# Performance work log

Measured on AMD Instinct MI355X. Metric: run time of the kernel, lower is better.

The kernel has to match this reference:

```python
import jax, jax.numpy as jnp
import numpy as np

N = 50000          # nodes
E = 400000         # edges
F = 128            # num_embeddings
NUM_TYPES = 100    # num_atoms (embedding vocab)
CUTOFF = 5.0
N_RBF = 20


def _silu(x):
    return x * jax.nn.sigmoid(x)


def setup_inputs() -> dict:
    key = jax.random.key(0)
    ks = jax.random.split(key, 16)
    pos = jax.random.normal(ks[0], (N, 3), dtype=jnp.float32) * 3.0
    z = jax.random.randint(ks[1], (N,), 0, NUM_TYPES)
    dst = jax.random.randint(ks[2], (E,), 0, N)
    # ensure src != dst so distances are nonzero
    src = (dst + 1 + jax.random.randint(ks[3], (E,), 0, N - 1)) % N
    def lin(k, fan_in, fan_out):
        kw, kb = jax.random.split(k)
        lim = 1.0 / np.sqrt(fan_in)
        W = jax.random.uniform(kw, (fan_out, fan_in), minval=-lim, maxval=lim, dtype=jnp.float32)
        b = jax.random.uniform(kb, (fan_out,), minval=-lim, maxval=lim, dtype=jnp.float32)
        return W, b
    emb_table = jax.random.normal(ks[4], (NUM_TYPES, F), dtype=jnp.float32)
    Wp1, bp1 = lin(ks[5], F, F)
    Wp2, bp2 = lin(ks[6], F, 3 * F)
    Ww, bw = lin(ks[7], N_RBF, 3 * F)
    Wu, bu = lin(ks[8], F, F)
    Wv, bv = lin(ks[9], F, F)
    Wu1, bu1 = lin(ks[10], 2 * F, F)
    Wu2, bu2 = lin(ks[11], F, 3 * F)
    return dict(pos=pos, emb_table=emb_table,
                Wp1=Wp1, bp1=bp1, Wp2=Wp2, bp2=bp2, Ww=Ww, bw=bw,
                Wu=Wu, bu=bu, Wv=Wv, bv=bv, Wu1=Wu1, bu1=bu1, Wu2=Wu2, bu2=bu2,
                z=z, src=src, dst=dst)


def painn_forward(pos, emb_table, Wp1, bp1, Wp2, bp2, Ww, bw, Wu, bu, Wv, bv,
                  Wu1, bu1, Wu2, bu2, z, src, dst):
    s = emb_table[z]                                  # [N,F] scalar features
    v = jnp.zeros((N, F, 3), dtype=s.dtype)          # equivariant features

    # ---- message block ----
    phi = _silu(s @ Wp1.T + bp1) @ Wp2.T + bp2       # [N,3F]
    rel = pos[dst] - pos[src]                        # [E,3]
    d = jnp.maximum(jnp.linalg.norm(rel, axis=-1), 1e-9)  # [E]
    n = jnp.arange(1, N_RBF + 1, dtype=jnp.float32)
    rbf = jnp.sin(n * jnp.pi * d[:, None] / CUTOFF) / d[:, None]   # [E,20]
    Wf = rbf @ Ww.T + bw                             # [E,3F]
    split = phi[src] * Wf                            # [E,3F] gated message
    ds = jax.ops.segment_sum(split[:, :F], dst, num_segments=N)    # [N,F]
    direction = rel / d[:, None]                     # [E,3]
    dv_e = v[src] * split[:, F:2 * F, None] + split[:, 2 * F:, None] * direction[:, None, :]  # [E,F,3]
    dv = jax.ops.segment_sum(dv_e, dst, num_segments=N)            # [N,F,3]
    s = s + ds
    v = v + dv

    # ---- update block ----
    U = jnp.einsum('nfc,gf->ngc', v, Wu) + bu[:, None]   # [N,F,3]
    V = jnp.einsum('nfc,gf->ngc', v, Wv) + bv[:, None]   # [N,F,3]
    Vn = jnp.linalg.norm(V, axis=-1)                     # [N,F]
    h = jnp.concatenate([s, Vn], axis=-1)                # [N,2F]
    a = _silu(h @ Wu1.T + bu1) @ Wu2.T + bu2             # [N,3F]
    dv2 = U * a[:, :F, None]                             # [N,F,3]
    ds2 = a[:, F:2 * F] + jnp.sum(U * V, axis=-1) * a[:, 2 * F:]   # [N,F]
    return s + ds2, v + dv2


def reference(pos, emb_table, Wp1, bp1, Wp2, bp2, Ww, bw, Wu, bu, Wv, bv,
              Wu1, bu1, Wu2, bu2, z, src, dst):
    return painn_forward(pos, emb_table, Wp1, bp1, Wp2, bp2, Ww, bw, Wu, bu,
                         Wv, bv, Wu1, bu1, Wu2, bu2, z, src, dst)
```

## Files before the change

kernel.cpp:

```cpp
#include <hip/hip_runtime.h>

#define NN 50000
#define EE 400000
#define FF 128
#define NRBF 20
#define MAXDEG 64
#define PI_OVER_CUT 0.6283185307179586f

typedef _Float16 h8 __attribute__((ext_vector_type(8)));
typedef float    f4 __attribute__((ext_vector_type(4)));

union pk32 { unsigned int u; _Float16 h[2]; };

__global__ __launch_bounds__(256) void k_zero(int* __restrict__ counts) {
    int i = blockIdx.x * 256 + threadIdx.x;
    if (i < NN) counts[i] = 0;
}

__global__ __launch_bounds__(256) void k_bucket(const int* __restrict__ dst,
                                                int* __restrict__ counts,
                                                int* __restrict__ slots) {
    int e = blockIdx.x * 256 + threadIdx.x;
    if (e < EE) {
        int n = dst[e];
        int slot = atomicAdd(&counts[n], 1);
        if (slot < MAXDEG) slots[n * MAXDEG + slot] = e;
    }
}

__global__ __launch_bounds__(256) void k_wconv(
    const float* __restrict__ Wu, const float* __restrict__ Wv,
    const float* __restrict__ Wu1, const float* __restrict__ Wu2,
    const float* __restrict__ Wp1, const float* __restrict__ Wp2,
    const float* __restrict__ Ww, const float* __restrict__ bw,
    _Float16* __restrict__ Wuh, _Float16* __restrict__ Wvh,
    _Float16* __restrict__ Wu1h, _Float16* __restrict__ Wu2h,
    _Float16* __restrict__ Wp1h, _Float16* __restrict__ Wp2h,
    _Float16* __restrict__ Wwh32)
{
    int i = blockIdx.x * 256 + threadIdx.x;
    if (i < 16384) { Wuh[i] = (_Float16)Wu[i]; Wvh[i] = (_Float16)Wv[i];
                     Wp1h[i] = (_Float16)Wp1[i]; }
    if (i < 32768) { Wu1h[i] = (_Float16)Wu1[i]; }
    if (i < 49152) { Wu2h[i] = (_Float16)Wu2[i]; Wp2h[i] = (_Float16)Wp2[i]; }
    if (i < 8192) {
        int col = i >> 5, k = i & 31;
        int sr = col < 128 ? col : col + 128;
        _Float16 v = (_Float16)0.f;
        if (k < 20)       v = (_Float16)Ww[sr * NRBF + k];
        else if (k == 20) v = (_Float16)bw[sr];
        Wwh32[i] = v;
    }
}

__global__ __launch_bounds__(256) void k_node_phi_mfma(
    const float* __restrict__ emb, const int* __restrict__ z,
    const _Float16* __restrict__ Wp1h, const float* __restrict__ bp1,
    const _Float16* __restrict__ Wp2h, const float* __restrict__ bp2,
    unsigned int* __restrict__ phi_pk, float* __restrict__ s_io)
{
    __shared__ _Float16 Ss[32 * 128];
    __shared__ _Float16 H1s[32 * 128];

    const int t    = threadIdx.x;
    const int lane = t & 63;
    const int w    = t >> 6;
    const int lr   = lane & 15;
    const int lq   = lane >> 4;
    const int n0   = blockIdx.x * 32;
    const f4 z4 = {0.f, 0.f, 0.f, 0.f};

    for (int i = t; i < 512; i += 256) {
        int n = i >> 4, gr = i & 15;
        int nn = n0 + n; if (nn > NN - 1) nn = NN - 1;
        const float* sp = &emb[(size_t)z[nn] * FF + gr * 8];
        float4 aa = *(const float4*)sp;
        float4 bb = *(const float4*)(sp + 4);
        h8 hv;
        hv[0] = (_Float16)aa.x; hv[1] = (_Float16)aa.y;
        hv[2] = (_Float16)aa.z; hv[3] = (_Float16)aa.w;
        hv[4] = (_Float16)bb.x; hv[5] = (_Float16)bb.y;
        hv[6] = (_Float16)bb.z; hv[7] = (_Float16)bb.w;
        *(h8*)&Ss[(n * 16 + (gr ^ (n & 15))) * 8] = hv;
        float* op = &s_io[(size_t)nn * FF + gr * 8];
        *(float4*)op       = aa;
        *(float4*)(op + 4) = bb;
    }
    __syncthreads();

    f4 acc1[2][2];
    #pragma unroll
    for (int a = 0; a < 2; ++a)
        #pragma unroll
        for (int m = 0; m < 2; ++m) acc1[a][m] = z4;
    {
        const _Float16* bb = Wp1h + (size_t)lr * 128 + lq * 8;
        #pragma unroll
        for (int g2 = 0; g2 < 2; ++g2) {
            h8 bf[4];
            #pragma unroll
            for (int ks = 0; ks < 4; ++ks)
                bf[ks] = *(const h8*)(bb + ((2 * w + g2) * 16) * 128 + ks * 32);
            #pragma unroll
            for (int mt = 0; mt < 2; ++mt) {
                const int r = mt * 16 + lr;
                #pragma unroll
                for (int ks = 0; ks < 4; ++ks) {
                    h8 af = *(const h8*)&Ss[(r * 16 + ((ks * 4 + lq) ^ (r & 15))) * 8];
                    acc1[g2][mt] = __builtin_amdgcn_mfma_f32_16x16x32_f16(
                        af, bf[ks], acc1[g2][mt], 0, 0, 0);
                }
            }
        }
    }
    #pragma unroll
    for (int g2 = 0; g2 < 2; ++g2) {
        const int g = (2 * w + g2) * 16 + lr;
        const float b1 = bp1[g];
        #pragma unroll
        for (int mt = 0; mt < 2; ++mt)
            #pragma unroll
            for (int r = 0; r < 4; ++r) {
                float x = acc1[g2][mt][r] + b1;
                float y = x / (1.f + __expf(-x));
                int n = mt * 16 + lq * 4 + r;
                H1s[(n * 16 + ((g >> 3) ^ (n & 15))) * 8 + (g & 7)] = (_Float16)y;
            }
    }
    __syncthreads();

    f4 accS[2][2], accV[2][2];
    #pragma unroll
    for (int a = 0; a < 2; ++a)
        #pragma unroll
        for (int m = 0; m < 2; ++m) { accS[a][m] = z4; accV[a][m] = z4; }
    {
        const _Float16* bbs = Wp2h + (size_t)lr * 128 + lq * 8;
        const _Float16* bbv = Wp2h + (size_t)(256 + lr) * 128 + lq * 8;
        #pragma unroll
        for (int g2 = 0; g2 < 2; ++g2) {
            h8 bfs[4], bfv[4];
            #pragma unroll
            for (int ks = 0; ks < 4; ++ks) {
                bfs[ks] = *(const h8*)(bbs + ((2 * w + g2) * 16) * 128 + ks * 32);
                bfv[ks] = *(const h8*)(bbv + ((2 * w + g2) * 16) * 128 + ks * 32);
            }
            #pragma unroll
            for (int mt = 0; mt < 2; ++mt) {
                const int r = mt * 16 + lr;
                #pragma unroll
                for (int ks = 0; ks < 4; ++ks) {
                    h8 af = *(const h8*)&H1s[(r * 16 + ((ks * 4 + lq) ^ (r & 15))) * 8];
                    accS[g2][mt] = __builtin_amdgcn_mfma_f32_16x16x32_f16(
                        af, bfs[ks], accS[g2][mt], 0, 0, 0);
                    accV[g2][mt] = __builtin_amdgcn_mfma_f32_16x16x32_f16(
                        af, bfv[ks], accV[g2][mt], 0, 0, 0);
                }
            }
        }
    }
    #pragma unroll
    for (int g2 = 0; g2 < 2; ++g2) {
        const int g = (2 * w + g2) * 16 + lr;
        const float bsa = bp2[g], bva = bp2[256 + g];
        #pragma unroll
        for (int mt = 0; mt < 2; ++mt)
            #pragma unroll
            for (int r = 0; r < 4; ++r) {
                int n = mt * 16 + lq * 4 + r;
                int nn = n0 + n;
                if (nn < NN) {
                    pk32 pk;
                    pk.h[0] = (_Float16)(accS[g2][mt][r] + bsa);
                    pk.h[1] = (_Float16)(accV[g2][mt][r] + bva);
                    phi_pk[(size_t)nn * FF + g] = pk.u;
                }
            }
    }
}

__global__ __launch_bounds__(128) void k_edge_mfma(
    const float* __restrict__ pos,
    const _Float16* __restrict__ Wwh32,
    const int* __restrict__ src,
    const int* __restrict__ counts, const int* __restrict__ slots,
    const unsigned int* __restrict__ phi_pk,
    float* __restrict__ s_io,
    _Float16* __restrict__ xg)
{
    __shared__ _Float16 A[16 * 32];
    __shared__ float dirs[16][4];
    __shared__ float dls[16];
    __shared__ unsigned int wf[16 * 130];

    const int t    = threadIdx.x;
    const int lane = t & 63;
    const int w    = t >> 6;
    const int lr   = lane & 15;
    const int lq   = lane >> 4;
    const int n    = blockIdx.x;
    const f4 z4 = {0.f, 0.f, 0.f, 0.f};

    h8 bf[8];
    #pragma unroll
    for (int j = 0; j < 8; ++j)
        bf[j] = *(const h8*)&Wwh32[(size_t)((w * 8 + j) * 16 + lr) * 32 + lq * 8];

    const float px = pos[3 * n], py = pos[3 * n + 1], pz = pos[3 * n + 2];

    int deg = counts[n];
    deg = deg > MAXDEG ? MAXDEG : deg;

    float acc_s = 0.f, av0 = 0.f, av1 = 0.f, av2 = 0.f;

    for (int t0 = 0; t0 < deg; t0 += 16) {
        const int degT = (deg - t0) < 16 ? (deg - t0) : 16;
        __syncthreads();
        if (t < degT) {
            int e  = slots[n * MAXDEG + t0 + t];
            int sI = src[e];
            float rx = px - pos[3 * sI];
            float ry = py - pos[3 * sI + 1];
            float rz = pz - pos[3 * sI + 2];
            float d = sqrtf(rx * rx + ry * ry + rz * rz);
            d = fmaxf(d, 1e-9f);
            float di = 1.f / d;
            dirs[t][0] = rx * di;
            dirs[t][1] = ry * di;
            dirs[t][2] = rz * di;
            dirs[t][3] = __int_as_float(sI);
            dls[t] = d;
        }
        __syncthreads();
        {
            const int m = t & 15, kk = t >> 4;
            float d  = dls[m];
            float di = 1.f / d;
            float v0 = __sinf((float)(kk + 1) * PI_OVER_CUT * d) * di;
            float v1 = __sinf((float)(kk + 9) * PI_OVER_CUT * d) * di;
            float v2;
            if (kk < 4)       v2 = __sinf((float)(kk + 17) * PI_OVER_CUT * d) * di;
            else if (kk == 4) v2 = 1.0f;
            else              v2 = 0.f;
            #define STO(K, V) A[m * 32 + (((K) >> 3) ^ (m & 3)) * 8 + ((K) & 7)] = (_Float16)(V)
            STO(kk,      v0);
            STO(kk + 8,  v1);
            STO(kk + 16, v2);
            STO(kk + 24, 0.f);
            #undef STO
        }
        __syncthreads();
        {
            h8 af = *(const h8*)&A[(lr * 4 + (lq ^ (lr & 3))) * 8];
            #pragma unroll
            for (int j = 0; j < 8; ++j) {
                f4 dd = __builtin_amdgcn_mfma_f32_16x16x32_f16(af, bf[j], z4, 0, 0, 0);
                #pragma unroll
                for (int r = 0; r < 4; ++r) {
                    int m = lq * 4 + r;
                    ((_Float16*)&wf[m * 130 + j * 16 + lr])[w] = (_Float16)dd[r];
                }
            }
        }
        __syncthreads();
        for (int m = 0; m < degT; ++m) {
            float4 dir = *(const float4*)&dirs[m][0];
            int sI = __builtin_amdgcn_readfirstlane(__float_as_int(dir.w));
            pk32 ph, wfu;
            ph.u  = phi_pk[(size_t)sI * FF + t];
            wfu.u = wf[m * 130 + t];
            float ps = (float)ph.h[0] * (float)wfu.h[0];
            float pv = (float)ph.h[1] * (float)wfu.h[1];
            acc_s += ps;
            av0 = fmaf(pv, dir.x, av0);
            av1 = fmaf(pv, dir.y, av1);
            av2 = fmaf(pv, dir.z, av2);
        }
    }

    size_t gi = (size_t)n * FF + t;
    s_io[gi] += acc_s;
    xg[((size_t)n * 3 + 0) * FF + t] = (_Float16)av0;
    xg[((size_t)n * 3 + 1) * FF + t] = (_Float16)av1;
    xg[((size_t)n * 3 + 2) * FF + t] = (_Float16)av2;
}

__global__ __launch_bounds__(256) void k_update_mfma(
    const _Float16* __restrict__ xg,
    const _Float16* __restrict__ Wuh, const _Float16* __restrict__ Wvh,
    const _Float16* __restrict__ Wu1h, const _Float16* __restrict__ Wu2h,
    const float* __restrict__ bu, const float* __restrict__ bv,
    const float* __restrict__ bu1, const float* __restrict__ bu2,
    float* __restrict__ s_io, float* __restrict__ v_io)
{
    __shared__ _Float16 Xs[96 * 128];
    __shared__ _Float16 Hs[32 * 256];
    __shared__ _Float16 H1s[32 * 128];

    const int t    = threadIdx.x;
    const int lane = t & 63;
    const int w    = t >> 6;
    const int lr   = lane & 15;
    const int lq   = lane >> 4;
    const int n0   = blockIdx.x * 32;
    const f4 z4 = {0.f, 0.f, 0.f, 0.f};

    for (int i = t; i < 1536; i += 256) {
        int row = i >> 4, gr = i & 15;
        int n = row & 31, c = row >> 5;
        int nn = n0 + n; if (nn > NN - 1) nn = NN - 1;
        uint4 d = *(const uint4*)&xg[((size_t)nn * 3 + c) * FF + gr * 8];
        *(uint4*)&Xs[(row * 16 + (gr ^ (row & 15))) * 8] = d;
    }
    for (int i = t; i < 512; i += 256) {
        int n = i >> 4, gr = i & 15;
        int nn = n0 + n; if (nn > NN - 1) nn = NN - 1;
        const float* sp = &s_io[(size_t)nn * FF + gr * 8];
        float4 aa = *(const float4*)sp;
        float4 bb = *(const float4*)(sp + 4);
        h8 hv;
        hv[0] = (_Float16)aa.x; hv[1] = (_Float16)aa.y;
        hv[2] = (_Float16)aa.z; hv[3] = (_Float16)aa.w;
        hv[4] = (_Float16)bb.x; hv[5] = (_Float16)bb.y;
        hv[6] = (_Float16)bb.z; hv[7] = (_Float16)bb.w;
        *(h8*)&Hs[(n * 32 + (gr ^ (n & 15))) * 8] = hv;
    }
    __syncthreads();

    f4 accU[2][6], accV[2][6];
    #pragma unroll
    for (int a = 0; a < 2; ++a)
        #pragma unroll
        for (int m = 0; m < 6; ++m) { accU[a][m] = z4; accV[a][m] = z4; }

    {
        const _Float16* bb = Wuh + (size_t)lr * 128 + lq * 8;
        h8 bfr[2][4];
        #pragma unroll
        for (int g2 = 0; g2 < 2; ++g2)
            #pragma unroll
            for (int ks = 0; ks < 4; ++ks)
                bfr[g2][ks] = *(const h8*)(bb + ((2 * w + g2) * 16) * 128 + ks * 32);
        #pragma unroll
        for (int mt = 0; mt < 6; ++mt) {
            const int r = mt * 16 + lr;
            h8 af[4];
            #pragma unroll
            for (int ks = 0; ks < 4; ++ks)
                af[ks] = *(const h8*)&Xs[(r * 16 + ((ks * 4 + lq) ^ (r & 15))) * 8];
            #pragma unroll
            for (int g2 = 0; g2 < 2; ++g2)
                #pragma unroll
                for (int ks = 0; ks < 4; ++ks)
                    accU[g2][mt] = __builtin_amdgcn_mfma_f32_16x16x32_f16(
                        af[ks], bfr[g2][ks], accU[g2][mt], 0, 0, 0);
        }
    }
    {
        const _Float16* bb = Wvh + (size_t)lr * 128 + lq * 8;
        h8 bfr[2][4];
        #pragma unroll
        for (int g2 = 0; g2 < 2; ++g2)
            #pragma unroll
            for (int ks = 0; ks < 4; ++ks)
                bfr[g2][ks] = *(const h8*)(bb + ((2 * w + g2) * 16) * 128 + ks * 32);
        #pragma unroll
        for (int mt = 0; mt < 6; ++mt) {
            const int r = mt * 16 + lr;
            h8 af[4];
            #pragma unroll
            for (int ks = 0; ks < 4; ++ks)
                af[ks] = *(const h8*)&Xs[(r * 16 + ((ks * 4 + lq) ^ (r & 15))) * 8];
            #pragma unroll
            for (int g2 = 0; g2 < 2; ++g2)
                #pragma unroll
                for (int ks = 0; ks < 4; ++ks)
                    accV[g2][mt] = __builtin_amdgcn_mfma_f32_16x16x32_f16(
                        af[ks], bfr[g2][ks], accV[g2][mt], 0, 0, 0);
        }
    }

    float uvr[2][2][4];
    #pragma unroll
    for (int g2 = 0; g2 < 2; ++g2) {
        const int g = (2 * w + g2) * 16 + lr;
        const float bU = bu[g], bV = bv[g];
        #pragma unroll
        for (int p = 0; p < 2; ++p) {
            #pragma unroll
            for (int r = 0; r < 4; ++r) {
                float Ux = accU[g2][0 + p][r] + bU;
                float Uy = accU[g2][2 + p][r] + bU;
                float Uz = accU[g2][4 + p][r] + bU;
                float Vx = accV[g2][0 + p][r] + bV;
                float Vy = accV[g2][2 + p][r] + bV;
                float Vz = accV[g2][4 + p][r] + bV;
                accU[g2][0 + p][r] = Ux;
                accU[g2][2 + p][r] = Uy;
                accU[g2][4 + p][r] = Uz;
                uvr[g2][p][r] = Ux * Vx + Uy * Vy + Uz * Vz;
                float vn = sqrtf(Vx * Vx + Vy * Vy + Vz * Vz);
                int n = p * 16 + lq * 4 + r;
                int gr = 16 + (g >> 3);
                Hs[(n * 32 + (gr ^ (n & 15))) * 8 + (g & 7)] = (_Float16)vn;
            }
        }
    }
    __syncthreads();

    f4 acc2[2][2];
    #pragma unroll
    for (int a = 0; a < 2; ++a)
        #pragma unroll
        for (int m = 0; m < 2; ++m) acc2[a][m] = z4;
    {
        const _Float16* bb = Wu1h + (size_t)lr * 256 + lq * 8;
        #pragma unroll
        for (int g2 = 0; g2 < 2; ++g2) {
            h8 bfr[8];
            #pragma unroll
            for (int ks = 0; ks < 8; ++ks)
                bfr[ks] = *(const h8*)(bb + ((2 * w + g2) * 16) * 256 + ks * 32);
            #pragma unroll
            for (int mt = 0; mt < 2; ++mt) {
                const int r = mt * 16 + lr;
                #pragma unroll
                for (int ks = 0; ks < 8; ++ks) {
                    h8 af = *(const h8*)&Hs[(r * 32 + ((ks * 4 + lq) ^ (r & 15))) * 8];
                    acc2[g2][mt] = __builtin_amdgcn_mfma_f32_16x16x32_f16(
                        af, bfr[ks], acc2[g2][mt], 0, 0, 0);
                }
            }
        }
    }
    #pragma unroll
    for (int g2 = 0; g2 < 2; ++g2) {
        const int g = (2 * w + g2) * 16 + lr;
        const float b1 = bu1[g];
        #pragma unroll
        for (int mt = 0; mt < 2; ++mt)
            #pragma unroll
            for (int r = 0; r < 4; ++r) {
                float x = acc2[g2][mt][r] + b1;
                float y = x / (1.f + __expf(-x));
                int n = mt * 16 + lq * 4 + r;
                int gr = g >> 3;
                H1s[(n * 16 + (gr ^ (n & 15))) * 8 + (g & 7)] = (_Float16)y;
            }
    }
    __syncthreads();

    f4 acc3[3][2][2];
    #pragma unroll
    for (int a = 0; a < 3; ++a)
        #pragma unroll
        for (int b = 0; b < 2; ++b)
            #pragma unroll
            for (int m = 0; m < 2; ++m) acc3[a][b][m] = z4;
    {
        const _Float16* bb = Wu2h + (size_t)lr * 128 + lq * 8;
        #pragma unroll
        for (int ai = 0; ai < 3; ++ai)
            #pragma unroll
            for (int g2 = 0; g2 < 2; ++g2) {
                const int jt = ai * 8 + 2 * w + g2;
                h8 bfr[4];
                #pragma unroll
                for (int ks = 0; ks < 4; ++ks)
                    bfr[ks] = *(const h8*)(bb + (size_t)(jt * 16) * 128 + ks * 32);
                #pragma unroll
                for (int mt = 0; mt < 2; ++mt) {
                    const int r = mt * 16 + lr;
                    #pragma unroll
                    for (int ks = 0; ks < 4; ++ks) {
                        h8 af = *(const h8*)&H1s[(r * 16 + ((ks * 4 + lq) ^ (r & 15))) * 8];
                        acc3[ai][g2][mt] = __builtin_amdgcn_mfma_f32_16x16x32_f16(
                            af, bfr[ks], acc3[ai][g2][mt], 0, 0, 0);
                    }
                }
            }
    }

    #pragma unroll
    for (int g2 = 0; g2 < 2; ++g2) {
        const int g = (2 * w + g2) * 16 + lr;
        const float b1 = bu2[g], b2 = bu2[128 + g], b3 = bu2[256 + g];
        #pragma unroll
        for (int p = 0; p < 2; ++p)
            #pragma unroll
            for (int r = 0; r < 4; ++r) {
                int n = p * 16 + lq * 4 + r;
                int nn = n0 + n;
                if (nn < NN) {
                    float a1 = acc3[0][g2][p][r] + b1;
                    float a2 = acc3[1][g2][p][r] + b2;
                    float a3 = acc3[2][g2][p][r] + b3;
                    size_t gi = (size_t)nn * FF + g;
                    float s1 = (float)Hs[(n * 32 + ((g >> 3) ^ (n & 15))) * 8 + (g & 7)];
                    s_io[gi] = s1 + a2 + uvr[g2][p][r] * a3;
                    float vx = (float)Xs[((0 * 32 + n) * 16 + ((g >> 3) ^ (n & 15))) * 8 + (g & 7)];
                    float vy = (float)Xs[((1 * 32 + n) * 16 + ((g >> 3) ^ (n & 15))) * 8 + (g & 7)];
                    float vz = (float)Xs[((2 * 32 + n) * 16 + ((g >> 3) ^ (n & 15))) * 8 + (g & 7)];
                    v_io[gi * 3 + 0] = vx + accU[g2][0 + p][r] * a1;
                    v_io[gi * 3 + 1] = vy + accU[g2][2 + p][r] * a1;
                    v_io[gi * 3 + 2] = vz + accU[g2][4 + p][r] * a1;
                }
            }
    }
}

extern "C" void kernel_launch(void* const* d_in, const int* in_sizes, int n_in,
                              void* d_out, int out_size, void* d_ws, size_t ws_size,
                              hipStream_t stream)
{
    const float* pos = (const float*)d_in[0];
    const float* emb = (const float*)d_in[1];
    const float* Wp1 = (const float*)d_in[2];
    const float* bp1 = (const float*)d_in[3];
    const float* Wp2 = (const float*)d_in[4];
    const float* bp2 = (const float*)d_in[5];
    const float* Ww  = (const float*)d_in[6];
    const float* bw  = (const float*)d_in[7];
    const float* Wu  = (const float*)d_in[8];
    const float* bu  = (const float*)d_in[9];
    const float* Wv  = (const float*)d_in[10];
    const float* bv  = (const float*)d_in[11];
    const float* Wu1 = (const float*)d_in[12];
    const float* bu1 = (const float*)d_in[13];
    const float* Wu2 = (const float*)d_in[14];
    const float* bu2 = (const float*)d_in[15];
    const int* z   = (const int*)d_in[16];
    const int* src = (const int*)d_in[17];
    const int* dst = (const int*)d_in[18];

    float* s_io = (float*)d_out;
    float* v_io = (float*)d_out + (size_t)NN * FF;

    char* ws = (char*)d_ws;
    unsigned int* phi_pk = (unsigned int*)ws;
    _Float16* xg    = (_Float16*)(phi_pk + (size_t)NN * FF);
    _Float16* Wuh   = xg + (size_t)NN * 3 * FF;
    _Float16* Wvh   = Wuh  + 128 * 128;
    _Float16* Wu1h  = Wvh  + 128 * 128;
    _Float16* Wu2h  = Wu1h + 128 * 256;
    _Float16* Wp1h  = Wu2h + 384 * 128;
    _Float16* Wp2h  = Wp1h + 128 * 128;
    _Float16* Wwh32 = Wp2h + 384 * 128;
    int* counts = (int*)(Wwh32 + 256 * 32);
    int* slots  = counts + NN;

    k_zero  <<<(NN + 255) / 256, 256, 0, stream>>>(counts);
    k_bucket<<<(EE + 255) / 256, 256, 0, stream>>>(dst, counts, slots);
    k_wconv <<<192, 256, 0, stream>>>(Wu, Wv, Wu1, Wu2, Wp1, Wp2, Ww, bw,
                                      Wuh, Wvh, Wu1h, Wu2h, Wp1h, Wp2h, Wwh32);
    k_node_phi_mfma<<<(NN + 31) / 32, 256, 0, stream>>>(emb, z, Wp1h, bp1,
                                                        Wp2h, bp2,
                                                        phi_pk, s_io);
    k_edge_mfma<<<NN, 128, 0, stream>>>(pos, Wwh32, src, counts, slots,
                                        phi_pk, s_io, xg);
    k_update_mfma<<<(NN + 31) / 32, 256, 0, stream>>>(xg, Wuh, Wvh, Wu1h, Wu2h,
                                                      bu, bv, bu1, bu2, s_io, v_io);
}
```

Before: 396.1 us.

## Make edge kernel persistent with software prefetch of next node's edge data

The edge kernel now launches a fixed grid of 3072 blocks that loop over nodes with a grid stride. While each node is processed, the block prefetches the next node's degree, position, first 16 slot indices, source ids and source positions into registers. For the first tile it batches all 16 phi gathers into registers before accumulating, which exposes more memory-level parallelism. This is meant to hide gather latency and the per-block weight-load cost, at the price of higher register pressure and duplicated code.

After: 399.0 us. No clear change (+0.7%).

```diff
diff --git a/kernel.cpp b/kernel.cpp
--- a/kernel.cpp
+++ b/kernel.cpp
@@ -198,7 +198,6 @@
     const int w    = t >> 6;
     const int lr   = lane & 15;
     const int lq   = lane >> 4;
-    const int n    = blockIdx.x;
     const f4 z4 = {0.f, 0.f, 0.f, 0.f};
 
     h8 bf[8];
@@ -206,32 +205,70 @@
     for (int j = 0; j < 8; ++j)
         bf[j] = *(const h8*)&Wwh32[(size_t)((w * 8 + j) * 16 + lr) * 32 + lq * 8];
 
-    const float px = pos[3 * n], py = pos[3 * n + 1], pz = pos[3 * n + 2];
-
-    int deg = counts[n];
-    deg = deg > MAXDEG ? MAXDEG : deg;
-
-    float acc_s = 0.f, av0 = 0.f, av1 = 0.f, av2 = 0.f;
-
-    for (int t0 = 0; t0 < deg; t0 += 16) {
-        const int degT = (deg - t0) < 16 ? (deg - t0) : 16;
+    const int G = gridDim.x;
+
+    int   deg_pf = 0;
+    float dpx = 0.f, dpy = 0.f, dpz = 0.f;
+    int   sI_pf = 0;
+    float spx = 0.f, spy = 0.f, spz = 0.f;
+    {
+        int n1 = blockIdx.x;
+        if (n1 < NN) {
+            deg_pf = counts[n1];
+            dpx = pos[3 * n1]; dpy = pos[3 * n1 + 1]; dpz = pos[3 * n1 + 2];
+            if (t < 16) {
+                int e = slots[n1 * MAXDEG + t];
+                if ((unsigned)e >= EE) e = 0;
+                sI_pf = src[e];
+                spx = pos[3 * sI_pf];
+                spy = pos[3 * sI_pf + 1];
+                spz = pos[3 * sI_pf + 2];
+            }
+        }
+    }
+
+    for (int n = blockIdx.x; n < NN; n += G) {
+        int deg = deg_pf; deg = deg > MAXDEG ? MAXDEG : deg;
+        const float px = dpx, py = dpy, pz = dpz;
+        const int   sIc = sI_pf;
+        const float sxc = spx, syc = spy, szc = spz;
+
+        float acc_s = 0.f, av0 = 0.f, av1 = 0.f, av2 = 0.f;
+        const size_t gi = (size_t)n * FF + t;
+
         __syncthreads();
-        if (t < degT) {
-            int e  = slots[n * MAXDEG + t0 + t];
-            int sI = src[e];
-            float rx = px - pos[3 * sI];
-            float ry = py - pos[3 * sI + 1];
-            float rz = pz - pos[3 * sI + 2];
+        const int degT0 = deg < 16 ? deg : 16;
+        if (t < degT0) {
+            float rx = px - sxc, ry = py - syc, rz = pz - szc;
             float d = sqrtf(rx * rx + ry * ry + rz * rz);
             d = fmaxf(d, 1e-9f);
             float di = 1.f / d;
             dirs[t][0] = rx * di;
             dirs[t][1] = ry * di;
             dirs[t][2] = rz * di;
-            dirs[t][3] = __int_as_float(sI);
+            dirs[t][3] = __int_as_float(sIc);
             dls[t] = d;
         }
+        float s_old = s_io[gi];
         __syncthreads();
+
+        {
+            int n2 = n + G;
+            deg_pf = 0;
+            if (n2 < NN) {
+                deg_pf = counts[n2];
+                dpx = pos[3 * n2]; dpy = pos[3 * n2 + 1]; dpz = pos[3 * n2 + 2];
+                if (t < 16) {
+                    int e = slots[n2 * MAXDEG + t];
+                    if ((unsigned)e >= EE) e = 0;
+                    sI_pf = src[e];
+                    spx = pos[3 * sI_pf];
+                    spy = pos[3 * sI_pf + 1];
+                    spz = pos[3 * sI_pf + 2];
+                }
+            }
+        }
+
         {
             const int m = t & 15, kk = t >> 4;
             float d  = dls[m];
@@ -263,26 +300,101 @@
             }
         }
         __syncthreads();
-        for (int m = 0; m < degT; ++m) {
-            float4 dir = *(const float4*)&dirs[m][0];
-            int sI = __builtin_amdgcn_readfirstlane(__float_as_int(dir.w));
-            pk32 ph, wfu;
-            ph.u  = phi_pk[(size_t)sI * FF + t];
-            wfu.u = wf[m * 130 + t];
-            float ps = (float)ph.h[0] * (float)wfu.h[0];
-            float pv = (float)ph.h[1] * (float)wfu.h[1];
-            acc_s += ps;
-            av0 = fmaf(pv, dir.x, av0);
-            av1 = fmaf(pv, dir.y, av1);
-            av2 = fmaf(pv, dir.z, av2);
-        }
-    }
-
-    size_t gi = (size_t)n * FF + t;
-    s_io[gi] += acc_s;
-    xg[((size_t)n * 3 + 0) * FF + t] = (_Float16)av0;
-    xg[((size_t)n * 3 + 1) * FF + t] = (_Float16)av1;
-    xg[((size_t)n * 3 + 2) * FF + t] = (_Float16)av2;
+        {
+            unsigned int phr[16];
+            #pragma unroll
+            for (int m = 0; m < 16; ++m) {
+                int sIm = __float_as_int(dirs[m][3]);
+                unsigned int v = 0u;
+                if (m < degT0) v = phi_pk[(size_t)sIm * FF + t];
+                phr[m] = v;
+            }
+            #pragma unroll
+            for (int m = 0; m < 16; ++m) {
+                if (m < degT0) {
+                    pk32 ph, wfu;
+                    ph.u  = phr[m];
+                    wfu.u = wf[m * 130 + t];
+                    float ps = (float)ph.h[0] * (float)wfu.h[0];
+                    float pv = (float)ph.h[1] * (float)wfu.h[1];
+                    acc_s += ps;
+                    av0 = fmaf(pv, dirs[m][0], av0);
+                    av1 = fmaf(pv, dirs[m][1], av1);
+                    av2 = fmaf(pv, dirs[m][2], av2);
+                }
+            }
+        }
+
+        for (int t0 = 16; t0 < deg; t0 += 16) {
+            const int degT = (deg - t0) < 16 ? (deg - t0) : 16;
+            __syncthreads();
+            if (t < degT) {
+                int e  = slots[n * MAXDEG + t0 + t];
+                int sI = src[e];
+                float rx = px - pos[3 * sI];
+                float ry = py - pos[3 * sI + 1];
+                float rz = pz - pos[3 * sI + 2];
+                float d = sqrtf(rx * rx + ry * ry + rz * rz);
+                d = fmaxf(d, 1e-9f);
+                float di = 1.f / d;
+                dirs[t][0] = rx * di;
+                dirs[t][1] = ry * di;
+                dirs[t][2] = rz * di;
+                dirs[t][3] = __int_as_float(sI);
+                dls[t] = d;
+            }
+            __syncthreads();
+            {
+                const int m = t & 15, kk = t >> 4;
+                float d  = dls[m];
+                float di = 1.f / d;
+                float v0 = __sinf((float)(kk + 1) * PI_OVER_CUT * d) * di;
+                float v1 = __sinf((float)(kk + 9) * PI_OVER_CUT * d) * di;
+                float v2;
+                if (kk < 4)       v2 = __sinf((float)(kk + 17) * PI_OVER_CUT * d) * di;
+                else if (kk == 4) v2 = 1.0f;
+                else              v2 = 0.f;
+                #define STO(K, V) A[m * 32 + (((K) >> 3) ^ (m & 3)) * 8 + ((K) & 7)] = (_Float16)(V)
+                STO(kk,      v0);
+                STO(kk + 8,  v1);
+                STO(kk + 16, v2);
+                STO(kk + 24, 0.f);
+                #undef STO
+            }
+            __syncthreads();
+            {
+                h8 af = *(const h8*)&A[(lr * 4 + (lq ^ (lr & 3))) * 8];
+                #pragma unroll
+                for (int j = 0; j < 8; ++j) {
+                    f4 dd = __builtin_amdgcn_mfma_f32_16x16x32_f16(af, bf[j], z4, 0, 0, 0);
+                    #pragma unroll
+                    for (int r = 0; r < 4; ++r) {
+                        int m = lq * 4 + r;
+                        ((_Float16*)&wf[m * 130 + j * 16 + lr])[w] = (_Float16)dd[r];
+                    }
+                }
+            }
+            __syncthreads();
+            for (int m = 0; m < degT; ++m) {
+                float4 dir = *(const float4*)&dirs[m][0];
+                int sI = __builtin_amdgcn_readfirstlane(__float_as_int(dir.w));
+                pk32 ph, wfu;
+                ph.u  = phi_pk[(size_t)sI * FF + t];
+                wfu.u = wf[m * 130 + t];
+                float ps = (float)ph.h[0] * (float)wfu.h[0];
+                float pv = (float)ph.h[1] * (float)wfu.h[1];
+                acc_s += ps;
+                av0 = fmaf(pv, dir.x, av0);
+                av1 = fmaf(pv, dir.y, av1);
+                av2 = fmaf(pv, dir.z, av2);
+            }
+        }
+
+        s_io[gi] = s_old + acc_s;
+        xg[((size_t)n * 3 + 0) * FF + t] = (_Float16)av0;
+        xg[((size_t)n * 3 + 1) * FF + t] = (_Float16)av1;
+        xg[((size_t)n * 3 + 2) * FF + t] = (_Float16)av2;
+    }
 }
 
 __global__ __launch_bounds__(256) void k_update_mfma(
@@ -556,8 +668,8 @@
     k_node_phi_mfma<<<(NN + 31) / 32, 256, 0, stream>>>(emb, z, Wp1h, bp1,
                                                         Wp2h, bp2,
                                                         phi_pk, s_io);
-    k_edge_mfma<<<NN, 128, 0, stream>>>(pos, Wwh32, src, counts, slots,
-                                        phi_pk, s_io, xg);
+    k_edge_mfma<<<3072, 128, 0, stream>>>(pos, Wwh32, src, counts, slots,
+                                          phi_pk, s_io, xg);
     k_update_mfma<<<(NN + 31) / 32, 256, 0, stream>>>(xg, Wuh, Wvh, Wu1h, Wu2h,
                                                       bu, bv, bu1, bu2, s_io, v_io);
 }
```
